# Kernel tuning notes

Hardware: AMD Instinct MI355X
Metric: run time of the kernel (lower is better)

## Reference

```python
import jax, jax.numpy as jnp
import numpy as np

NUM_GROUPS = 32
EPS = 1e-5


def setup_inputs() -> dict:
    key = jax.random.key(0)
    ks = jax.random.split(key, 6)
    B, C, H, W = 8, 128, 64, 64
    d = C // 8
    x = jax.random.normal(ks[0], (B, C, H, W), dtype=jnp.float32)
    # conv 1x1 weights stored as [out_ch, in_ch]; scaled like torch kaiming-uniform-ish
    s = 1.0 / np.sqrt(C)
    return {
        "x": x,
        "gn_w": jnp.ones((C,), jnp.float32),
        "gn_b": jnp.zeros((C,), jnp.float32),
        "q_w": jax.random.normal(ks[1], (d, C), jnp.float32) * s,
        "q_b": jnp.zeros((d,), jnp.float32),
        "k_w": jax.random.normal(ks[2], (d, C), jnp.float32) * s,
        "k_b": jnp.zeros((d,), jnp.float32),
        "v_w": jax.random.normal(ks[3], (C, C), jnp.float32) * s,
        "v_b": jnp.zeros((C,), jnp.float32),
        "p_w": jax.random.normal(ks[4], (C, C), jnp.float32) * s,
        "p_b": jnp.zeros((C,), jnp.float32),
    }


def _group_norm(x, w, b):
    B, C, H, W = x.shape
    g = NUM_GROUPS
    xr = x.reshape(B, g, C // g, H, W)
    mu = xr.mean(axis=(2, 3, 4), keepdims=True)
    var = xr.var(axis=(2, 3, 4), keepdims=True)
    xn = ((xr - mu) * jax.lax.rsqrt(var + EPS)).reshape(B, C, H, W)
    return xn * w[None, :, None, None] + b[None, :, None, None]


def reference(x, gn_w, gn_b, q_w, q_b, k_w, k_b, v_w, v_b, p_w, p_b):
    B, C, H, W = x.shape
    N = H * W
    h_ = _group_norm(x, gn_w, gn_b)            # [B,C,H,W]
    hf = h_.reshape(B, C, N)                   # flatten spatial
    # 1x1 convs == channel matmuls
    q = jnp.einsum('dc,bcn->bnd', q_w, hf) + q_b[None, None, :]   # [B,N,d]
    k = jnp.einsum('dc,bcn->bnd', k_w, hf) + k_b[None, None, :]   # [B,N,d]
    v = jnp.einsum('ec,bcn->ben', v_w, hf) + v_b[None, :, None]   # [B,C,N]
    d = q.shape[-1]
    scale = jnp.asarray(int(d) ** (-0.5), x.dtype)
    attn = jnp.einsum('bid,bjd->bij', q, k) * scale               # [B,N,N]
    attn = jax.nn.softmax(attn, axis=-1)
    a = jnp.einsum('bcj,bij->bci', v, attn)                       # [B,C,N]
    proj = jnp.einsum('ec,bcn->ben', p_w, a) + p_b[None, :, None]
    return x + proj.reshape(B, C, H, W)
```

## Files before the change

### kernel.cpp

```cpp
#include <hip/hip_runtime.h>
#include <math.h>


typedef short v8s __attribute__((ext_vector_type(8)));
typedef float v16f __attribute__((ext_vector_type(16)));

__device__ __forceinline__ unsigned short f2bf_rne(float f) {
  unsigned u = __float_as_uint(f);
  u += 0x7fffu + ((u >> 16) & 1u);
  return (unsigned short)(u >> 16);
}

__device__ __forceinline__ v8s mk8(unsigned a, unsigned b, unsigned c, unsigned d) {
  union { unsigned u[4]; v8s s; } x;
  x.u[0] = a; x.u[1] = b; x.u[2] = c; x.u[3] = d;
  return x.s;
}

__device__ __forceinline__ unsigned pack_trunc(float hi, float lo) {
  return __builtin_amdgcn_perm(__float_as_uint(hi), __float_as_uint(lo), 0x07060302u);
}

#define VT(b, n, c) (((((size_t)(b) * 256 + ((n) >> 4)) << 7) + (c)) * 16 + ((n) & 15))

#define WSB_MURS   0u
#define WSB_WCATB  4096u
#define WSB_BCAT   49152u
#define WSB_PWB    65536u
#define WSB_QBF    131072u
#define WSB_KBF    1310720u
#define WSB_VBF    2621440u
#define WSB_ABF    11534336u

__global__ void prep_kernel(const float* __restrict__ qw, const float* __restrict__ qb,
                            const float* __restrict__ kw, const float* __restrict__ kb,
                            const float* __restrict__ vw, const float* __restrict__ vb,
                            const float* __restrict__ pw,
                            unsigned short* __restrict__ wcatb, float* __restrict__ bcat,
                            unsigned short* __restrict__ pwb) {
  const float qs = 0.36067376022224085f;
  int idx = blockIdx.x * 256 + threadIdx.x;
  if (idx < 160 * 128) {
    int o = idx >> 7, c = idx & 127;
    float val;
    if (o < 16)       val = qw[o * 128 + c] * qs;
    else if (o < 32)  val = kw[(o - 16) * 128 + c];
    else              val = vw[(o - 32) * 128 + c];
    wcatb[idx] = f2bf_rne(val);
  } else if (idx < 160 * 128 + 160) {
    int o = idx - 160 * 128;
    bcat[o] = (o < 16) ? qb[o] * qs : (o < 32) ? kb[o - 16] : vb[o - 32];
  } else if (idx < 160 * 128 + 160 + 128 * 128) {
    int j = idx - (160 * 128 + 160);
    pwb[j] = f2bf_rne(pw[j]);
  }
}

__global__ __launch_bounds__(512)
void gn_stats_kernel(const float* __restrict__ x, float* __restrict__ mu_rs) {
  const int id = blockIdx.x;
  const int bg = (id & 7) * 32 + (id >> 3);
  const float4* xp = (const float4*)(x + (size_t)bg * 16384);
  float s = 0.f, ss = 0.f;
#pragma unroll
  for (int u = 0; u < 8; ++u) {
    int i = threadIdx.x + u * 512;
    float4 v = xp[i];
    s  += v.x + v.y + v.z + v.w;
    ss += v.x * v.x + v.y * v.y + v.z * v.z + v.w * v.w;
  }
  for (int off = 32; off > 0; off >>= 1) {
    s  += __shfl_down(s, off, 64);
    ss += __shfl_down(ss, off, 64);
  }
  __shared__ float red[16];
  int lane = threadIdx.x & 63, wid = threadIdx.x >> 6;
  if (lane == 0) { red[wid * 2] = s; red[wid * 2 + 1] = ss; }
  __syncthreads();
  if (threadIdx.x == 0) {
    float S = 0.f, SS = 0.f;
    for (int w = 0; w < 8; ++w) { S += red[w * 2]; SS += red[w * 2 + 1]; }
    float mu  = S * (1.0f / 16384.0f);
    float var = SS * (1.0f / 16384.0f) - mu * mu;
    float rs  = rsqrtf(var + 1e-5f);
    mu_rs[bg * 2]     = mu;
    mu_rs[bg * 2 + 1] = rs;
  }
}

__global__ __launch_bounds__(512)
void qkv_kernel(const float* __restrict__ x, const float* __restrict__ gnw,
                const float* __restrict__ gnb, const float* __restrict__ mu_rs,
                const unsigned short* __restrict__ wcatb, const float* __restrict__ bcat,
                unsigned short* __restrict__ qTb, unsigned short* __restrict__ kbf,
                unsigned short* __restrict__ vbf) {
  __shared__ float scs[128], shs[128], bsh[160];
  const int id = blockIdx.x;
  const int b = id & 7, nb = (id >> 3) << 6;
  const int t = threadIdx.x;
  const int w = t >> 6, lane = t & 63, h = lane >> 5, l = lane & 31;
  const int nsub = w & 1, og = w >> 1;
  if (t < 128) {
    float mu = mu_rs[(b * 32 + (t >> 2)) * 2];
    float rs = mu_rs[(b * 32 + (t >> 2)) * 2 + 1];
    float gw = gnw[t], gb = gnb[t];
    scs[t] = rs * gw; shs[t] = gb - mu * rs * gw;
  }
  if (t < 160) bsh[t] = bcat[t];
  __syncthreads();

  const int n = nb + nsub * 32 + l;
  const float* xb = x + ((size_t)b * 128 << 12);
  const int otbase = (og == 0) ? 0 : og + 1;

  float xv[64];
#pragma unroll
  for (int ks = 0; ks < 8; ++ks)
#pragma unroll
    for (int p = 0; p < 8; ++p)
      xv[ks * 8 + p] = xb[((size_t)(ks * 16 + 8 * h + p) << 12) + n];

  v16f acc[2];
#pragma unroll
  for (int a2 = 0; a2 < 2; ++a2)
#pragma unroll
    for (int r = 0; r < 16; ++r) acc[a2][r] = 0.f;

#pragma unroll
  for (int ks = 0; ks < 8; ++ks) {
    const int c0 = ks * 16 + 8 * h;
    unsigned fd[4];
#pragma unroll
    for (int p = 0; p < 4; ++p) {
      int ca = c0 + 2 * p;
      float h0 = xv[ks * 8 + 2 * p]     * scs[ca]     + shs[ca];
      float h1 = xv[ks * 8 + 2 * p + 1] * scs[ca + 1] + shs[ca + 1];
      fd[p] = (unsigned)f2bf_rne(h0) | ((unsigned)f2bf_rne(h1) << 16);
    }
    v8s bf = mk8(fd[0], fd[1], fd[2], fd[3]);
    {
      v8s af = *(const v8s*)(wcatb + (otbase * 32 + l) * 128 + ks * 16 + 8 * h);
      acc[0] = __builtin_amdgcn_mfma_f32_32x32x16_bf16(af, bf, acc[0], 0, 0, 0);
    }
    if (og == 0) {
      v8s af = *(const v8s*)(wcatb + (32 + l) * 128 + ks * 16 + 8 * h);
      acc[1] = __builtin_amdgcn_mfma_f32_32x32x16_bf16(af, bf, acc[1], 0, 0, 0);
    }
  }

  if (og == 0) {
    const size_t nqk = ((size_t)b * 4096 + n) << 4;
#pragma unroll
    for (int r = 0; r < 16; ++r) {
      int o = 4 * h + (r & 3) + 8 * (r >> 2);
      unsigned short bv = f2bf_rne(acc[0][r] + bsh[o]);
      if (o < 16) qTb[((size_t)(b * 16 + o) << 12) + n] = bv;
      else        kbf[nqk + o - 16] = bv;
    }
#pragma unroll
    for (int r = 0; r < 16; ++r) {
      int o = 32 + 4 * h + (r & 3) + 8 * (r >> 2);
      vbf[VT(b, n, o - 32)] = f2bf_rne(acc[1][r] + bsh[o]);
    }
  } else {
#pragma unroll
    for (int r = 0; r < 16; ++r) {
      int o = otbase * 32 + 4 * h + (r & 3) + 8 * (r >> 2);
      vbf[VT(b, n, o - 32)] = f2bf_rne(acc[0][r] + bsh[o]);
    }
  }
}

#define VS 24

__global__ __launch_bounds__(256)
void attn_kernel(const unsigned short* __restrict__ qTb,
                 const unsigned short* __restrict__ kbf,
                 const unsigned short* __restrict__ vbf,
                 unsigned short* __restrict__ abf) {
  __shared__ alignas(16) unsigned short smem[2][512 * VS];
  __shared__ float l_lds[64];

  const int id = blockIdx.x;
  const int b = id & 7, i0 = (id >> 3) << 6;
  const int t = threadIdx.x;
  const int w = t >> 6, lane = t & 63, h = lane >> 5, l = lane & 31;
  const int jsub = w & 1, ihalf = w >> 1;

  const unsigned short* kg = kbf + ((size_t)b << 16);
  const unsigned short* vg = vbf + ((size_t)b << 19);

  const int iglob = i0 + ihalf * 32 + l;
  unsigned qd[4];
#pragma unroll
  for (int e = 0; e < 4; ++e) {
    unsigned lo = qTb[((size_t)(b * 16 + 8 * h + 2 * e) << 12) + iglob];
    unsigned hi = qTb[((size_t)(b * 16 + 8 * h + 2 * e + 1) << 12) + iglob];
    qd[e] = lo | (hi << 16);
  }
  const v8s qf = mk8(qd[0], qd[1], qd[2], qd[3]);

  v16f zc;
#pragma unroll
  for (int r = 0; r < 16; ++r) zc[r] = 0.f;
  v16f acc[4];
#pragma unroll
  for (int ct = 0; ct < 4; ++ct)
#pragma unroll
    for (int r = 0; r < 16; ++r) acc[ct][r] = 0.f;
  float ls = 0.f;

  const int srow = w * 128 + (lane >> 1);
  const int sh16 = (lane & 1) * 8;

#pragma unroll
  for (int u = 0; u < 4; ++u) {
    v8s a = *(const v8s*)(vg + (size_t)(srow + 32 * u) * 16 + sh16);
    *(v8s*)(&smem[0][(srow + 32 * u) * VS + sh16]) = a;
  }
  if (t < 64) l_lds[t] = 0.f;
  __syncthreads();

  for (int tile = 0; tile < 64; ++tile) {
    const int tn = (tile + 1) & 63;
    unsigned short* const cur = smem[tile & 1];
    unsigned short* const nxt = smem[(tile + 1) & 1];

    v8s s[4];
#pragma unroll
    for (int u = 0; u < 4; ++u)
      s[u] = *(const v8s*)(vg + (size_t)tn * 8192 + (size_t)(srow + 32 * u) * 16 + sh16);

    v8s kf = *(const v8s*)(kg + (((size_t)(tile * 64 + jsub * 32 + l)) << 4) + 8 * h);

    v16f st = __builtin_amdgcn_mfma_f32_32x32x16_bf16(kf, qf, zc, 0, 0, 0);
    float pe[16];
#pragma unroll
    for (int r = 0; r < 16; ++r) { pe[r] = __builtin_amdgcn_exp2f(st[r]); ls += pe[r]; }
    unsigned G[8];
#pragma unroll
    for (int g = 0; g < 4; ++g) {
      G[2 * g]     = pack_trunc(pe[4 * g + 1], pe[4 * g]);
      G[2 * g + 1] = pack_trunc(pe[4 * g + 3], pe[4 * g + 2]);
    }
    unsigned S0 = h ? G[0] : G[2], S1 = h ? G[1] : G[3];
    unsigned S2 = h ? G[4] : G[6], S3 = h ? G[5] : G[7];
    unsigned R0 = (unsigned)__shfl_xor((int)S0, 32, 64);
    unsigned R1 = (unsigned)__shfl_xor((int)S1, 32, 64);
    unsigned R2 = (unsigned)__shfl_xor((int)S2, 32, 64);
    unsigned R3 = (unsigned)__shfl_xor((int)S3, 32, 64);
    v8s pf0 = h ? mk8(R0, R1, G[2], G[3]) : mk8(G[0], G[1], R0, R1);
    v8s pf1 = h ? mk8(R2, R3, G[6], G[7]) : mk8(G[4], G[5], R2, R3);

#pragma unroll
    for (int ct = 0; ct < 4; ++ct) {
      v8s vf0 = *(const v8s*)(&cur[((jsub * 2) * 128 + ct * 32 + l) * VS + 8 * h]);
      v8s vf1 = *(const v8s*)(&cur[((jsub * 2 + 1) * 128 + ct * 32 + l) * VS + 8 * h]);
      acc[ct] = __builtin_amdgcn_mfma_f32_32x32x16_bf16(vf0, pf0, acc[ct], 0, 0, 0);
      acc[ct] = __builtin_amdgcn_mfma_f32_32x32x16_bf16(vf1, pf1, acc[ct], 0, 0, 0);
    }

#pragma unroll
    for (int u = 0; u < 4; ++u)
      *(v8s*)(&nxt[(srow + 32 * u) * VS + sh16]) = s[u];

    __syncthreads();
  }

  atomicAdd(&l_lds[ihalf * 32 + l], ls);
  __syncthreads();

  float* const ov = (float*)smem;
  if (jsub == 1) {
#pragma unroll
    for (int ct = 0; ct < 4; ++ct)
#pragma unroll
      for (int q = 0; q < 4; ++q) {
        float4 v4 = {acc[ct][4 * q], acc[ct][4 * q + 1],
                     acc[ct][4 * q + 2], acc[ct][4 * q + 3]};
        *(float4*)&ov[((ct * 2 + ihalf) * 32 + l) * 36 + 4 * h + 8 * q] = v4;
      }
  }
  __syncthreads();
  if (jsub == 0) {
    const float li = 1.f / l_lds[ihalf * 32 + l];
#pragma unroll
    for (int ct = 0; ct < 4; ++ct) {
#pragma unroll
      for (int q = 0; q < 4; ++q) {
        float4 v4 = *(float4*)&ov[((ct * 2 + ihalf) * 32 + l) * 36 + 4 * h + 8 * q];
        acc[ct][4 * q]     += v4.x;
        acc[ct][4 * q + 1] += v4.y;
        acc[ct][4 * q + 2] += v4.z;
        acc[ct][4 * q + 3] += v4.w;
      }
#pragma unroll
      for (int r = 0; r < 16; ++r) {
        int c = ct * 32 + 4 * h + (r & 3) + 8 * (r >> 2);
        abf[((size_t)(b * 128 + c) << 12) + (size_t)(i0 + ihalf * 32 + l)] =
            f2bf_rne(acc[ct][r] * li);
      }
    }
  }
}

__global__ __launch_bounds__(512)
void proj_kernel(const unsigned short* __restrict__ abf, const unsigned short* __restrict__ pwb,
                 const float* __restrict__ pb, const float* __restrict__ x,
                 float* __restrict__ out) {
  __shared__ float pbs[128];
  const int id = blockIdx.x;
  const int b = id & 7, nb = (id >> 3) << 6;
  const int t = threadIdx.x;
  const int w = t >> 6, lane = t & 63, h = lane >> 5, l = lane & 31;
  const int nsub = w & 1, ot = w >> 1;
  if (t < 128) pbs[t] = pb[t];
  __syncthreads();

  const int n = nb + nsub * 32 + l;
  const unsigned short* ab = abf + (((size_t)b * 128) << 12);

  unsigned short av[64];
#pragma unroll
  for (int ks = 0; ks < 8; ++ks)
#pragma unroll
    for (int p = 0; p < 8; ++p)
      av[ks * 8 + p] = ab[((size_t)(ks * 16 + 8 * h + p) << 12) + n];

  v16f acc;
#pragma unroll
  for (int r = 0; r < 16; ++r) acc[r] = 0.f;

#pragma unroll
  for (int ks = 0; ks < 8; ++ks) {
    unsigned fd[4];
#pragma unroll
    for (int p = 0; p < 4; ++p)
      fd[p] = (unsigned)av[ks * 8 + 2 * p] | ((unsigned)av[ks * 8 + 2 * p + 1] << 16);
    v8s bf = mk8(fd[0], fd[1], fd[2], fd[3]);
    v8s af = *(const v8s*)(pwb + (ot * 32 + l) * 128 + ks * 16 + 8 * h);
    acc = __builtin_amdgcn_mfma_f32_32x32x16_bf16(af, bf, acc, 0, 0, 0);
  }

#pragma unroll
  for (int r = 0; r < 16; ++r) {
    int e = ot * 32 + 4 * h + (r & 3) + 8 * (r >> 2);
    size_t idx = ((size_t)(b * 128 + e) << 12) + n;
    out[idx] = acc[r] + pbs[e] + x[idx];
  }
}

extern "C" void kernel_launch(void* const* d_in, const int* in_sizes, int n_in,
                              void* d_out, int out_size, void* d_ws, size_t ws_size,
                              hipStream_t stream) {
  const float* x   = (const float*)d_in[0];
  const float* gnw = (const float*)d_in[1];
  const float* gnb = (const float*)d_in[2];
  const float* qw  = (const float*)d_in[3];
  const float* qb  = (const float*)d_in[4];
  const float* kw  = (const float*)d_in[5];
  const float* kb  = (const float*)d_in[6];
  const float* vw  = (const float*)d_in[7];
  const float* vb  = (const float*)d_in[8];
  const float* pw  = (const float*)d_in[9];
  const float* pb  = (const float*)d_in[10];
  float* out = (float*)d_out;
  char* ws = (char*)d_ws;

  float* mu_rs = (float*)(ws + WSB_MURS);
  unsigned short* wcatb = (unsigned short*)(ws + WSB_WCATB);
  float* bcat = (float*)(ws + WSB_BCAT);
  unsigned short* pwb = (unsigned short*)(ws + WSB_PWB);
  unsigned short* qTb = (unsigned short*)(ws + WSB_QBF);
  unsigned short* kbf = (unsigned short*)(ws + WSB_KBF);
  unsigned short* vbf = (unsigned short*)(ws + WSB_VBF);
  unsigned short* abf = (unsigned short*)(ws + WSB_ABF);

  hipLaunchKernelGGL(prep_kernel, dim3(145), dim3(256), 0, stream,
                     qw, qb, kw, kb, vw, vb, pw, wcatb, bcat, pwb);
  hipLaunchKernelGGL(gn_stats_kernel, dim3(256), dim3(512), 0, stream, x, mu_rs);
  hipLaunchKernelGGL(qkv_kernel, dim3(512), dim3(512), 0, stream,
                     x, gnw, gnb, mu_rs, wcatb, bcat, qTb, kbf, vbf);
  hipLaunchKernelGGL(attn_kernel, dim3(512), dim3(256), 0, stream,
                     qTb, kbf, vbf, abf);
  hipLaunchKernelGGL(proj_kernel, dim3(512), dim3(512), 0, stream,
                     abf, pwb, pb, x, out);
}
```

Measured before the change: 166.8 us.

## Use async global-to-LDS copies for V tiles and fuse weight prep into GN stats

The attention kernel now streams V tiles straight into LDS with global_load_lds 16-byte copies instead of loading through registers and storing, and drops the padded row stride. This frees VGPRs and the explicit store instructions, at the cost of possible LDS bank conflicts on the now unpadded reads. The epilogue reduction is split into two passes so it needs less LDS. The weight-prep kernel is merged into the GN stats kernel, removing one launch.

```diff
diff --git a/kernel.cpp b/kernel.cpp
--- a/kernel.cpp
+++ b/kernel.cpp
@@ -19,6 +19,12 @@
 
 __device__ __forceinline__ unsigned pack_trunc(float hi, float lo) {
   return __builtin_amdgcn_perm(__float_as_uint(hi), __float_as_uint(lo), 0x07060302u);
+}
+
+__device__ __forceinline__ void cp16_async(const unsigned short* g, unsigned short* l) {
+  __builtin_amdgcn_global_load_lds(
+      (const __attribute__((address_space(1))) unsigned int*)g,
+      (__attribute__((address_space(3))) unsigned int*)l, 16, 0, 0);
 }
 
 #define VT(b, n, c) (((((size_t)(b) * 256 + ((n) >> 4)) << 7) + (c)) * 16 + ((n) & 15))
@@ -32,33 +38,33 @@
 #define WSB_VBF    2621440u
 #define WSB_ABF    11534336u
 
-__global__ void prep_kernel(const float* __restrict__ qw, const float* __restrict__ qb,
-                            const float* __restrict__ kw, const float* __restrict__ kb,
-                            const float* __restrict__ vw, const float* __restrict__ vb,
-                            const float* __restrict__ pw,
-                            unsigned short* __restrict__ wcatb, float* __restrict__ bcat,
-                            unsigned short* __restrict__ pwb) {
-  const float qs = 0.36067376022224085f;
-  int idx = blockIdx.x * 256 + threadIdx.x;
-  if (idx < 160 * 128) {
-    int o = idx >> 7, c = idx & 127;
-    float val;
-    if (o < 16)       val = qw[o * 128 + c] * qs;
-    else if (o < 32)  val = kw[(o - 16) * 128 + c];
-    else              val = vw[(o - 32) * 128 + c];
-    wcatb[idx] = f2bf_rne(val);
-  } else if (idx < 160 * 128 + 160) {
-    int o = idx - 160 * 128;
-    bcat[o] = (o < 16) ? qb[o] * qs : (o < 32) ? kb[o - 16] : vb[o - 32];
-  } else if (idx < 160 * 128 + 160 + 128 * 128) {
-    int j = idx - (160 * 128 + 160);
-    pwb[j] = f2bf_rne(pw[j]);
-  }
-}
-
 __global__ __launch_bounds__(512)
-void gn_stats_kernel(const float* __restrict__ x, float* __restrict__ mu_rs) {
+void gnprep_kernel(const float* __restrict__ x, float* __restrict__ mu_rs,
+                   const float* __restrict__ qw, const float* __restrict__ qb,
+                   const float* __restrict__ kw, const float* __restrict__ kb,
+                   const float* __restrict__ vw, const float* __restrict__ vb,
+                   const float* __restrict__ pw,
+                   unsigned short* __restrict__ wcatb, float* __restrict__ bcat,
+                   unsigned short* __restrict__ pwb) {
   const int id = blockIdx.x;
+  {
+    const float qs = 0.36067376022224085f;
+    int idx = id * 512 + threadIdx.x;
+    if (idx < 160 * 128) {
+      int o = idx >> 7, c = idx & 127;
+      float val;
+      if (o < 16)       val = qw[o * 128 + c] * qs;
+      else if (o < 32)  val = kw[(o - 16) * 128 + c];
+      else              val = vw[(o - 32) * 128 + c];
+      wcatb[idx] = f2bf_rne(val);
+    } else if (idx < 160 * 128 + 160) {
+      int o = idx - 160 * 128;
+      bcat[o] = (o < 16) ? qb[o] * qs : (o < 32) ? kb[o - 16] : vb[o - 32];
+    } else if (idx < 160 * 128 + 160 + 128 * 128) {
+      int j = idx - (160 * 128 + 160);
+      pwb[j] = f2bf_rne(pw[j]);
+    }
+  }
   const int bg = (id & 7) * 32 + (id >> 3);
   const float4* xp = (const float4*)(x + (size_t)bg * 16384);
   float s = 0.f, ss = 0.f;
@@ -171,14 +177,12 @@
   }
 }
 
-#define VS 24
-
 __global__ __launch_bounds__(256)
 void attn_kernel(const unsigned short* __restrict__ qTb,
                  const unsigned short* __restrict__ kbf,
                  const unsigned short* __restrict__ vbf,
                  unsigned short* __restrict__ abf) {
-  __shared__ alignas(16) unsigned short smem[2][512 * VS];
+  __shared__ alignas(16) unsigned short smem[2][8192];
   __shared__ float l_lds[64];
 
   const int id = blockIdx.x;
@@ -210,15 +214,12 @@
     for (int r = 0; r < 16; ++r) acc[ct][r] = 0.f;
   float ls = 0.f;
 
-  const int srow = w * 128 + (lane >> 1);
-  const int sh16 = (lane & 1) * 8;
-
-#pragma unroll
-  for (int u = 0; u < 4; ++u) {
-    v8s a = *(const v8s*)(vg + (size_t)(srow + 32 * u) * 16 + sh16);
-    *(v8s*)(&smem[0][(srow + 32 * u) * VS + sh16]) = a;
-  }
   if (t < 64) l_lds[t] = 0.f;
+
+#pragma unroll
+  for (int u = 0; u < 4; ++u)
+    cp16_async(vg + (size_t)(w * 2048 + u * 512) + lane * 8,
+               &smem[0][w * 2048 + u * 512]);
   __syncthreads();
 
   for (int tile = 0; tile < 64; ++tile) {
@@ -226,10 +227,10 @@
     unsigned short* const cur = smem[tile & 1];
     unsigned short* const nxt = smem[(tile + 1) & 1];
 
-    v8s s[4];
 #pragma unroll
     for (int u = 0; u < 4; ++u)
-      s[u] = *(const v8s*)(vg + (size_t)tn * 8192 + (size_t)(srow + 32 * u) * 16 + sh16);
+      cp16_async(vg + (size_t)tn * 8192 + (w * 2048 + u * 512) + lane * 8,
+                 &nxt[w * 2048 + u * 512]);
 
     v8s kf = *(const v8s*)(kg + (((size_t)(tile * 64 + jsub * 32 + l)) << 4) + 8 * h);
 
@@ -254,53 +255,56 @@
 
 #pragma unroll
     for (int ct = 0; ct < 4; ++ct) {
-      v8s vf0 = *(const v8s*)(&cur[((jsub * 2) * 128 + ct * 32 + l) * VS + 8 * h]);
-      v8s vf1 = *(const v8s*)(&cur[((jsub * 2 + 1) * 128 + ct * 32 + l) * VS + 8 * h]);
+      v8s vf0 = *(const v8s*)(&cur[((jsub * 2) * 128 + ct * 32 + l) * 16 + 8 * h]);
+      v8s vf1 = *(const v8s*)(&cur[((jsub * 2 + 1) * 128 + ct * 32 + l) * 16 + 8 * h]);
       acc[ct] = __builtin_amdgcn_mfma_f32_32x32x16_bf16(vf0, pf0, acc[ct], 0, 0, 0);
       acc[ct] = __builtin_amdgcn_mfma_f32_32x32x16_bf16(vf1, pf1, acc[ct], 0, 0, 0);
     }
 
-#pragma unroll
-    for (int u = 0; u < 4; ++u)
-      *(v8s*)(&nxt[(srow + 32 * u) * VS + sh16]) = s[u];
-
     __syncthreads();
   }
 
   atomicAdd(&l_lds[ihalf * 32 + l], ls);
   __syncthreads();
-
   float* const ov = (float*)smem;
-  if (jsub == 1) {
-#pragma unroll
-    for (int ct = 0; ct < 4; ++ct)
-#pragma unroll
-      for (int q = 0; q < 4; ++q) {
-        float4 v4 = {acc[ct][4 * q], acc[ct][4 * q + 1],
-                     acc[ct][4 * q + 2], acc[ct][4 * q + 3]};
-        *(float4*)&ov[((ct * 2 + ihalf) * 32 + l) * 36 + 4 * h + 8 * q] = v4;
+  const float li = 1.f / l_lds[ihalf * 32 + l];
+#pragma unroll
+  for (int pass = 0; pass < 2; ++pass) {
+    const int cta = pass * 2, ctb = pass * 2 + 1;
+    if (jsub == 1) {
+#pragma unroll
+      for (int k = 0; k < 2; ++k) {
+        const int ct = pass * 2 + k;
+#pragma unroll
+        for (int q = 0; q < 4; ++q) {
+          float4 v4 = {acc[ct][4 * q], acc[ct][4 * q + 1],
+                       acc[ct][4 * q + 2], acc[ct][4 * q + 3]};
+          *(float4*)&ov[((k * 2 + ihalf) * 32 + l) * 36 + 4 * h + 8 * q] = v4;
+        }
       }
-  }
-  __syncthreads();
-  if (jsub == 0) {
-    const float li = 1.f / l_lds[ihalf * 32 + l];
-#pragma unroll
-    for (int ct = 0; ct < 4; ++ct) {
-#pragma unroll
-      for (int q = 0; q < 4; ++q) {
-        float4 v4 = *(float4*)&ov[((ct * 2 + ihalf) * 32 + l) * 36 + 4 * h + 8 * q];
-        acc[ct][4 * q]     += v4.x;
-        acc[ct][4 * q + 1] += v4.y;
-        acc[ct][4 * q + 2] += v4.z;
-        acc[ct][4 * q + 3] += v4.w;
+    }
+    __syncthreads();
+    if (jsub == 0) {
+#pragma unroll
+      for (int k = 0; k < 2; ++k) {
+        const int ct = pass * 2 + k;
+#pragma unroll
+        for (int q = 0; q < 4; ++q) {
+          float4 v4 = *(float4*)&ov[((k * 2 + ihalf) * 32 + l) * 36 + 4 * h + 8 * q];
+          acc[ct][4 * q]     += v4.x;
+          acc[ct][4 * q + 1] += v4.y;
+          acc[ct][4 * q + 2] += v4.z;
+          acc[ct][4 * q + 3] += v4.w;
+        }
+#pragma unroll
+        for (int r = 0; r < 16; ++r) {
+          int c = ct * 32 + 4 * h + (r & 3) + 8 * (r >> 2);
+          abf[((size_t)(b * 128 + c) << 12) + (size_t)(i0 + ihalf * 32 + l)] =
+              f2bf_rne(acc[ct][r] * li);
+        }
       }
-#pragma unroll
-      for (int r = 0; r < 16; ++r) {
-        int c = ct * 32 + 4 * h + (r & 3) + 8 * (r >> 2);
-        abf[((size_t)(b * 128 + c) << 12) + (size_t)(i0 + ihalf * 32 + l)] =
-            f2bf_rne(acc[ct][r] * li);
-      }
-    }
+    }
+    __syncthreads();
   }
 }
 
@@ -376,9 +380,8 @@
   unsigned short* vbf = (unsigned short*)(ws + WSB_VBF);
   unsigned short* abf = (unsigned short*)(ws + WSB_ABF);
 
-  hipLaunchKernelGGL(prep_kernel, dim3(145), dim3(256), 0, stream,
-                     qw, qb, kw, kb, vw, vb, pw, wcatb, bcat, pwb);
-  hipLaunchKernelGGL(gn_stats_kernel, dim3(256), dim3(512), 0, stream, x, mu_rs);
+  hipLaunchKernelGGL(gnprep_kernel, dim3(256), dim3(512), 0, stream,
+                     x, mu_rs, qw, qb, kw, kb, vw, vb, pw, wcatb, bcat, pwb);
   hipLaunchKernelGGL(qkv_kernel, dim3(512), dim3(512), 0, stream,
                      x, gnw, gnb, mu_rs, wcatb, bcat, qTb, kbf, vbf);
   hipLaunchKernelGGL(attn_kernel, dim3(512), dim3(256), 0, stream,
```

New measurement: 172.6 us. +3.4%, slower.

## Fuse output projection into attention kernel and merge weight prep with GN stats

Applied to the files above, without the earlier changes.

The attention output is now normalized and stored as bf16 into shared memory instead of global memory. Each of the four waves then runs the 128x128 projection MFMA for its 32-channel slice, adding bias and the residual directly. This removes the abf round trip through global memory and the separate proj launch. The weight-prep work is also folded into the GroupNorm stats kernel, dropping another launch. The cost is extra work and two more barriers at the tail of the attention kernel, plus more register pressure.

```diff
diff --git a/kernel.cpp b/kernel.cpp
--- a/kernel.cpp
+++ b/kernel.cpp
@@ -30,35 +30,34 @@
 #define WSB_QBF    131072u
 #define WSB_KBF    1310720u
 #define WSB_VBF    2621440u
-#define WSB_ABF    11534336u
-
-__global__ void prep_kernel(const float* __restrict__ qw, const float* __restrict__ qb,
-                            const float* __restrict__ kw, const float* __restrict__ kb,
-                            const float* __restrict__ vw, const float* __restrict__ vb,
-                            const float* __restrict__ pw,
-                            unsigned short* __restrict__ wcatb, float* __restrict__ bcat,
-                            unsigned short* __restrict__ pwb) {
-  const float qs = 0.36067376022224085f;
-  int idx = blockIdx.x * 256 + threadIdx.x;
-  if (idx < 160 * 128) {
-    int o = idx >> 7, c = idx & 127;
-    float val;
-    if (o < 16)       val = qw[o * 128 + c] * qs;
-    else if (o < 32)  val = kw[(o - 16) * 128 + c];
-    else              val = vw[(o - 32) * 128 + c];
-    wcatb[idx] = f2bf_rne(val);
-  } else if (idx < 160 * 128 + 160) {
-    int o = idx - 160 * 128;
-    bcat[o] = (o < 16) ? qb[o] * qs : (o < 32) ? kb[o - 16] : vb[o - 32];
-  } else if (idx < 160 * 128 + 160 + 128 * 128) {
-    int j = idx - (160 * 128 + 160);
-    pwb[j] = f2bf_rne(pw[j]);
-  }
-}
 
 __global__ __launch_bounds__(512)
-void gn_stats_kernel(const float* __restrict__ x, float* __restrict__ mu_rs) {
+void gnprep_kernel(const float* __restrict__ x, float* __restrict__ mu_rs,
+                   const float* __restrict__ qw, const float* __restrict__ qb,
+                   const float* __restrict__ kw, const float* __restrict__ kb,
+                   const float* __restrict__ vw, const float* __restrict__ vb,
+                   const float* __restrict__ pw,
+                   unsigned short* __restrict__ wcatb, float* __restrict__ bcat,
+                   unsigned short* __restrict__ pwb) {
   const int id = blockIdx.x;
+  {
+    const float qs = 0.36067376022224085f;
+    int idx = id * 512 + threadIdx.x;
+    if (idx < 160 * 128) {
+      int o = idx >> 7, c = idx & 127;
+      float val;
+      if (o < 16)       val = qw[o * 128 + c] * qs;
+      else if (o < 32)  val = kw[(o - 16) * 128 + c];
+      else              val = vw[(o - 32) * 128 + c];
+      wcatb[idx] = f2bf_rne(val);
+    } else if (idx < 160 * 128 + 160) {
+      int o = idx - 160 * 128;
+      bcat[o] = (o < 16) ? qb[o] * qs : (o < 32) ? kb[o - 16] : vb[o - 32];
+    } else if (idx < 160 * 128 + 160 + 128 * 128) {
+      int j = idx - (160 * 128 + 160);
+      pwb[j] = f2bf_rne(pw[j]);
+    }
+  }
   const int bg = (id & 7) * 32 + (id >> 3);
   const float4* xp = (const float4*)(x + (size_t)bg * 16384);
   float s = 0.f, ss = 0.f;
@@ -172,14 +171,19 @@
 }
 
 #define VS 24
+#define OTS 136
 
 __global__ __launch_bounds__(256)
 void attn_kernel(const unsigned short* __restrict__ qTb,
                  const unsigned short* __restrict__ kbf,
                  const unsigned short* __restrict__ vbf,
-                 unsigned short* __restrict__ abf) {
+                 const unsigned short* __restrict__ pwb,
+                 const float* __restrict__ pb,
+                 const float* __restrict__ x,
+                 float* __restrict__ out) {
   __shared__ alignas(16) unsigned short smem[2][512 * VS];
   __shared__ float l_lds[64];
+  __shared__ float pbs[128];
 
   const int id = blockIdx.x;
   const int b = id & 7, i0 = (id >> 3) << 6;
@@ -189,6 +193,8 @@
 
   const unsigned short* kg = kbf + ((size_t)b << 16);
   const unsigned short* vg = vbf + ((size_t)b << 19);
+
+  if (t < 128) pbs[t] = pb[t];
 
   const int iglob = i0 + ihalf * 32 + l;
   unsigned qd[4];
@@ -283,9 +289,8 @@
   }
   __syncthreads();
   if (jsub == 0) {
-    const float li = 1.f / l_lds[ihalf * 32 + l];
-#pragma unroll
-    for (int ct = 0; ct < 4; ++ct) {
+#pragma unroll
+    for (int ct = 0; ct < 4; ++ct)
 #pragma unroll
       for (int q = 0; q < 4; ++q) {
         float4 v4 = *(float4*)&ov[((ct * 2 + ihalf) * 32 + l) * 36 + 4 * h + 8 * q];
@@ -294,59 +299,43 @@
         acc[ct][4 * q + 2] += v4.z;
         acc[ct][4 * q + 3] += v4.w;
       }
-#pragma unroll
-      for (int r = 0; r < 16; ++r) {
+  }
+  __syncthreads();
+
+  unsigned short* const oT = (unsigned short*)smem;
+  if (jsub == 0) {
+    const float li = 1.f / l_lds[ihalf * 32 + l];
+    const int nrow = ihalf * 32 + l;
+#pragma unroll
+    for (int ct = 0; ct < 4; ++ct)
+#pragma unroll
+      for (int r = 0; r < 16; r += 2) {
         int c = ct * 32 + 4 * h + (r & 3) + 8 * (r >> 2);
-        abf[((size_t)(b * 128 + c) << 12) + (size_t)(i0 + ihalf * 32 + l)] =
-            f2bf_rne(acc[ct][r] * li);
+        unsigned dw = (unsigned)f2bf_rne(acc[ct][r] * li) |
+                      ((unsigned)f2bf_rne(acc[ct][r + 1] * li) << 16);
+        *(unsigned*)(&oT[nrow * OTS + c]) = dw;
       }
-    }
-  }
-}
-
-__global__ __launch_bounds__(512)
-void proj_kernel(const unsigned short* __restrict__ abf, const unsigned short* __restrict__ pwb,
-                 const float* __restrict__ pb, const float* __restrict__ x,
-                 float* __restrict__ out) {
-  __shared__ float pbs[128];
-  const int id = blockIdx.x;
-  const int b = id & 7, nb = (id >> 3) << 6;
-  const int t = threadIdx.x;
-  const int w = t >> 6, lane = t & 63, h = lane >> 5, l = lane & 31;
-  const int nsub = w & 1, ot = w >> 1;
-  if (t < 128) pbs[t] = pb[t];
-  __syncthreads();
-
-  const int n = nb + nsub * 32 + l;
-  const unsigned short* ab = abf + (((size_t)b * 128) << 12);
-
-  unsigned short av[64];
-#pragma unroll
-  for (int ks = 0; ks < 8; ++ks)
-#pragma unroll
-    for (int p = 0; p < 8; ++p)
-      av[ks * 8 + p] = ab[((size_t)(ks * 16 + 8 * h + p) << 12) + n];
-
-  v16f acc;
-#pragma unroll
-  for (int r = 0; r < 16; ++r) acc[r] = 0.f;
-
-#pragma unroll
-  for (int ks = 0; ks < 8; ++ks) {
-    unsigned fd[4];
-#pragma unroll
-    for (int p = 0; p < 4; ++p)
-      fd[p] = (unsigned)av[ks * 8 + 2 * p] | ((unsigned)av[ks * 8 + 2 * p + 1] << 16);
-    v8s bf = mk8(fd[0], fd[1], fd[2], fd[3]);
-    v8s af = *(const v8s*)(pwb + (ot * 32 + l) * 128 + ks * 16 + 8 * h);
-    acc = __builtin_amdgcn_mfma_f32_32x32x16_bf16(af, bf, acc, 0, 0, 0);
-  }
-
-#pragma unroll
-  for (int r = 0; r < 16; ++r) {
-    int e = ot * 32 + 4 * h + (r & 3) + 8 * (r >> 2);
-    size_t idx = ((size_t)(b * 128 + e) << 12) + n;
-    out[idx] = acc[r] + pbs[e] + x[idx];
+  }
+  __syncthreads();
+
+#pragma unroll
+  for (int nsub = 0; nsub < 2; ++nsub) {
+    v16f a2;
+#pragma unroll
+    for (int r = 0; r < 16; ++r) a2[r] = 0.f;
+#pragma unroll
+    for (int ks = 0; ks < 8; ++ks) {
+      v8s bf = *(const v8s*)(&oT[(nsub * 32 + l) * OTS + ks * 16 + 8 * h]);
+      v8s af = *(const v8s*)(pwb + (w * 32 + l) * 128 + ks * 16 + 8 * h);
+      a2 = __builtin_amdgcn_mfma_f32_32x32x16_bf16(af, bf, a2, 0, 0, 0);
+    }
+    const int n = i0 + nsub * 32 + l;
+#pragma unroll
+    for (int r = 0; r < 16; ++r) {
+      int e = w * 32 + 4 * h + (r & 3) + 8 * (r >> 2);
+      size_t idx = ((size_t)(b * 128 + e) << 12) + n;
+      out[idx] = a2[r] + pbs[e] + x[idx];
+    }
   }
 }
 
@@ -374,15 +363,11 @@
   unsigned short* qTb = (unsigned short*)(ws + WSB_QBF);
   unsigned short* kbf = (unsigned short*)(ws + WSB_KBF);
   unsigned short* vbf = (unsigned short*)(ws + WSB_VBF);
-  unsigned short* abf = (unsigned short*)(ws + WSB_ABF);
-
-  hipLaunchKernelGGL(prep_kernel, dim3(145), dim3(256), 0, stream,
-                     qw, qb, kw, kb, vw, vb, pw, wcatb, bcat, pwb);
-  hipLaunchKernelGGL(gn_stats_kernel, dim3(256), dim3(512), 0, stream, x, mu_rs);
+
+  hipLaunchKernelGGL(gnprep_kernel, dim3(256), dim3(512), 0, stream,
+                     x, mu_rs, qw, qb, kw, kb, vw, vb, pw, wcatb, bcat, pwb);
   hipLaunchKernelGGL(qkv_kernel, dim3(512), dim3(512), 0, stream,
                      x, gnw, gnb, mu_rs, wcatb, bcat, qTb, kbf, vbf);
   hipLaunchKernelGGL(attn_kernel, dim3(512), dim3(256), 0, stream,
-                     qTb, kbf, vbf, abf);
-  hipLaunchKernelGGL(proj_kernel, dim3(512), dim3(512), 0, stream,
-                     abf, pwb, pb, x, out);
-}
+                     qTb, kbf, vbf, pwb, pb, x, out);
+}
```

Measured after the change: 163.5 us. -2.0%, faster.
